# Performance work log

Measured on AMD Instinct MI355X. Metric: run time of the kernel, lower is better.

## Reference

```python
import jax, jax.numpy as jnp
import numpy as np

B, T, E, H = 2, 2048, 1024, 16
D = E // H            # head dim = 64
ROT = D // 2          # rotary_dim = 32 (only first half of head dim is rotated)
THETA = 10000.0


def _rope(x):
    # x: (B, H, T, D). Faithful to rotary_embedding_torch.rotate_queries_or_keys
    # with dim=ROT: rotate first ROT features, interleaved-pair style, pass rest.
    t = x.shape[-2]
    inv = 1.0 / (THETA ** (jnp.arange(0, ROT, 2, dtype=jnp.float32) / ROT))   # (ROT//2,)
    freqs = jnp.arange(t, dtype=jnp.float32)[:, None] * inv[None, :]          # (T, ROT//2)
    freqs = jnp.repeat(freqs, 2, axis=-1)                                      # (T, ROT)
    cos, sin = jnp.cos(freqs), jnp.sin(freqs)
    xr, xp = x[..., :ROT], x[..., ROT:]
    p = xr.reshape(*xr.shape[:-1], ROT // 2, 2)
    rot = jnp.stack((-p[..., 1], p[..., 0]), axis=-1).reshape(xr.shape)
    return jnp.concatenate([xr * cos + rot * sin, xp], axis=-1)


def setup_inputs() -> dict:
    key = jax.random.key(0)
    k1, k2, k3 = jax.random.split(key, 3)
    query = jax.random.normal(k1, (B, T, E), dtype=jnp.float32)
    inputs = {
        "query": query,
        "key": query,            # ignored (cross_attention=False)
        "value": query,          # ignored
        "padding_mask": jnp.ones((B, T), dtype=bool),
        "in_proj_weight": jax.random.uniform(k2, (3 * E, E), dtype=jnp.float32),
        "out_proj_weight": jax.random.normal(k3, (E, E), dtype=jnp.float32) * (E ** -0.5),
    }
    return inputs


def reference(query, key, value, padding_mask, in_proj_weight, out_proj_weight):
    # cross_attention=False: key/value are overwritten by query
    key = query
    value = query
    q = query @ in_proj_weight[:E].T
    k = key @ in_proj_weight[E:2 * E].T
    v = value @ in_proj_weight[2 * E:].T
    # NOTE: raw reshape (B,T,E)->(B,H,T,D), exactly as in the torch module
    q = q.reshape(B, H, T, D)
    k = k.reshape(B, H, T, D)
    v = v.reshape(B, H, T, D)
    q = _rope(q)
    k = _rope(k)   # causal self-attention path: rotate keys too
    causal = jnp.tril(jnp.ones((T, T), dtype=bool))                 # (T, T)
    mask = causal[None, None] & padding_mask[:, None, None, :]      # (B,1,T,T) -> broadcast over H
    scores = jnp.einsum("bhqd,bhkd->bhqk", q, k) / jnp.sqrt(jnp.float32(D))
    scores = jnp.where(mask, scores, -jnp.inf)
    attn = jax.nn.softmax(scores, axis=-1)
    x = jnp.einsum("bhqk,bhkd->bhqd", attn, v)
    x = x.reshape(B, T, E)      # raw reshape back, as in torch
    return x @ out_proj_weight.T
```

## Files before the change

kernel.cpp:

```cpp
#include <hip/hip_runtime.h>
#include <stdint.h>

#define T_ 2048
#define E_ 1024

typedef __attribute__((ext_vector_type(8))) __bf16 bf16x8;
typedef __attribute__((ext_vector_type(4))) float f32x4;

__device__ __forceinline__ void gload_lds16(const void* g, void* l) {
  __builtin_amdgcn_global_load_lds(
      (const __attribute__((address_space(1))) unsigned int*)g,
      (__attribute__((address_space(3))) unsigned int*)l, 16, 0, 0);
}

__global__ __launch_bounds__(256) void k_prep(const float4* __restrict__ q,
                                              ushort4* __restrict__ xh,
                                              ushort4* __restrict__ xl,
                                              const float4* __restrict__ win,
                                              ushort4* __restrict__ whh,
                                              ushort4* __restrict__ whl,
                                              const float4* __restrict__ wout,
                                              ushort4* __restrict__ wob,
                                              float2* __restrict__ cs) {
  const int b = blockIdx.x, tid = threadIdx.x;
  if (b < 7168) {
    const float4* src;
    ushort4 *hi, *lo;
    int i;
    if (b < 4096) { src = q; hi = xh; lo = xl; i = b * 256 + tid; }
    else          { src = win; hi = whh; lo = whl; i = (b - 4096) * 256 + tid; }
    float4 x = src[i];
    float xs[4] = {x.x, x.y, x.z, x.w};
    union { __bf16 bb[4]; ushort4 u; } H, L;
#pragma unroll
    for (int jj = 0; jj < 4; ++jj) {
      __bf16 h = (__bf16)xs[jj];
      H.bb[jj] = h;
      L.bb[jj] = (__bf16)(xs[jj] - (float)h);
    }
    hi[i] = H.u;
    lo[i] = L.u;
  } else if (b < 8192) {
    int i = (b - 7168) * 256 + tid;
    float4 x = wout[i];
    float xs[4] = {x.x, x.y, x.z, x.w};
    union { __bf16 bb[4]; ushort4 u; } H;
#pragma unroll
    for (int jj = 0; jj < 4; ++jj) H.bb[jj] = (__bf16)xs[jj];
    wob[i] = H.u;
  } else {
    int i = (b - 8192) * 256 + tid;
    int t = i >> 4, f = i & 15;
    double inv = pow(10000.0, -(double)f / 16.0);
    double ang = (double)t * inv;
    cs[i] = make_float2((float)cos(ang), (float)sin(ang));
  }
}

template <int EPI, bool HILO>
__global__ __launch_bounds__(256) void k_gemm(const __bf16* __restrict__ Ah,
                                              const __bf16* __restrict__ Al,
                                              const __bf16* __restrict__ Bh,
                                              const __bf16* __restrict__ Bl,
                                              int M, int N, int K,
                                              const float2* __restrict__ cs,
                                              __bf16* __restrict__ qhi,
                                              __bf16* __restrict__ qlo,
                                              __bf16* __restrict__ khi,
                                              __bf16* __restrict__ klo,
                                              __bf16* __restrict__ v16,
                                              float* __restrict__ C32) {
  __shared__ __align__(16) __bf16 AsH[128 * 32];
  __shared__ __align__(16) __bf16 BsH[128 * 32];
  __shared__ __align__(16) __bf16 AsL[HILO ? 128 * 32 : 4];
  __shared__ __align__(16) __bf16 BsL[HILO ? 128 * 32 : 4];
  const int tid = threadIdx.x, lane = tid & 63, w = tid >> 6;
  const int wm = w >> 1, wn = w & 1;
  const int g = lane >> 4, d = lane & 15;
  const int m0 = blockIdx.y * 128, n0 = blockIdx.x * 128;

  f32x4 acc[4][4];
#pragma unroll
  for (int i = 0; i < 4; ++i)
#pragma unroll
    for (int j = 0; j < 4; ++j) acc[i][j] = (f32x4)(0.0f);

  const int row0 = tid >> 2, kc = tid & 3;
  const int row1 = 64 + row0;

  for (int k0 = 0; k0 < K; k0 += 32) {
    __syncthreads();
    gload_lds16(Ah + (size_t)(m0 + row0) * K + k0 + kc * 8, &AsH[w * 512]);
    gload_lds16(Ah + (size_t)(m0 + row1) * K + k0 + kc * 8, &AsH[2048 + w * 512]);
    gload_lds16(Bh + (size_t)(n0 + row0) * K + k0 + kc * 8, &BsH[w * 512]);
    gload_lds16(Bh + (size_t)(n0 + row1) * K + k0 + kc * 8, &BsH[2048 + w * 512]);
    if constexpr (HILO) {
      gload_lds16(Al + (size_t)(m0 + row0) * K + k0 + kc * 8, &AsL[w * 512]);
      gload_lds16(Al + (size_t)(m0 + row1) * K + k0 + kc * 8, &AsL[2048 + w * 512]);
      gload_lds16(Bl + (size_t)(n0 + row0) * K + k0 + kc * 8, &BsL[w * 512]);
      gload_lds16(Bl + (size_t)(n0 + row1) * K + k0 + kc * 8, &BsL[2048 + w * 512]);
    }
    __syncthreads();
    bf16x8 ah[4], bh[4], al[4], bl[4];
#pragma unroll
    for (int i = 0; i < 4; ++i) {
      ah[i] = *(const bf16x8*)&AsH[(wm * 64 + i * 16 + d) * 32 + g * 8];
      bh[i] = *(const bf16x8*)&BsH[(wn * 64 + i * 16 + d) * 32 + g * 8];
      if constexpr (HILO) {
        al[i] = *(const bf16x8*)&AsL[(wm * 64 + i * 16 + d) * 32 + g * 8];
        bl[i] = *(const bf16x8*)&BsL[(wn * 64 + i * 16 + d) * 32 + g * 8];
      }
    }
#pragma unroll
    for (int i = 0; i < 4; ++i)
#pragma unroll
      for (int j = 0; j < 4; ++j) {
        acc[i][j] = __builtin_amdgcn_mfma_f32_16x16x32_bf16(ah[i], bh[j], acc[i][j], 0, 0, 0);
        if constexpr (HILO) {
          acc[i][j] = __builtin_amdgcn_mfma_f32_16x16x32_bf16(al[i], bh[j], acc[i][j], 0, 0, 0);
          acc[i][j] = __builtin_amdgcn_mfma_f32_16x16x32_bf16(ah[i], bl[j], acc[i][j], 0, 0, 0);
        }
      }
  }

#pragma unroll
  for (int i = 0; i < 4; ++i) {
    const int rbase = m0 + wm * 64 + i * 16 + g * 4;
#pragma unroll
    for (int j = 0; j < 4; ++j) {
      const int col = n0 + wn * 64 + j * 16 + d;
#pragma unroll
      for (int r = 0; r < 4; ++r) {
        const float vv = acc[i][j][r];
        const int row = rbase + r;
        if constexpr (EPI == 0) {
          const float xp = __shfl_xor(vv, 1);
          const int which = col >> 10;
          const int cl = col & 1023;
          const int d2 = cl & 63;
          const int t2 = (row & 127) * 16 + (cl >> 6);
          float y;
          if (d2 < 32) {
            const float2 cse = cs[t2 * 16 + (d2 >> 1)];
            y = (d2 & 1) ? (vv * cse.x + xp * cse.y) : (vv * cse.x - xp * cse.y);
          } else {
            y = vv;
          }
          if (which == 0) y *= 0.18033688011112042f;
          const __bf16 hi = (__bf16)y;
          const __bf16 lo = (__bf16)(y - (float)hi);
          const size_t off = (size_t)row * 1024 + cl;
          (which ? khi : qhi)[off] = hi;
          (which ? klo : qlo)[off] = lo;
        } else if constexpr (EPI == 1) {
          C32[(size_t)row * N + col] = vv;
        } else {
          v16[(size_t)row * N + col] = (__bf16)vv;
        }
      }
    }
  }
}

template <int EPI>
__global__ __launch_bounds__(256) void k_gemm64(const __bf16* __restrict__ Ah,
                                                const __bf16* __restrict__ Bh,
                                                int M, int N, int K,
                                                __bf16* __restrict__ v16,
                                                float* __restrict__ C32) {
  __shared__ __align__(16) __bf16 As[64 * 32];
  __shared__ __align__(16) __bf16 Bs[128 * 32];
  const int tid = threadIdx.x, lane = tid & 63, w = tid >> 6;
  const int g = lane >> 4, d = lane & 15;
  const int m0 = blockIdx.y * 64, n0 = blockIdx.x * 128;

  f32x4 acc[4][2];
#pragma unroll
  for (int i = 0; i < 4; ++i)
#pragma unroll
    for (int j = 0; j < 2; ++j) acc[i][j] = (f32x4)(0.0f);

  const int row0 = tid >> 2, kc = tid & 3;
  const int row1 = 64 + row0;

  for (int k0 = 0; k0 < K; k0 += 32) {
    __syncthreads();
    gload_lds16(Ah + (size_t)(m0 + row0) * K + k0 + kc * 8, &As[w * 512]);
    gload_lds16(Bh + (size_t)(n0 + row0) * K + k0 + kc * 8, &Bs[w * 512]);
    gload_lds16(Bh + (size_t)(n0 + row1) * K + k0 + kc * 8, &Bs[2048 + w * 512]);
    __syncthreads();
    bf16x8 ah[4], bh[2];
#pragma unroll
    for (int i = 0; i < 4; ++i) ah[i] = *(const bf16x8*)&As[(i * 16 + d) * 32 + g * 8];
#pragma unroll
    for (int j = 0; j < 2; ++j)
      bh[j] = *(const bf16x8*)&Bs[(w * 32 + j * 16 + d) * 32 + g * 8];
#pragma unroll
    for (int i = 0; i < 4; ++i)
#pragma unroll
      for (int j = 0; j < 2; ++j)
        acc[i][j] = __builtin_amdgcn_mfma_f32_16x16x32_bf16(ah[i], bh[j], acc[i][j], 0, 0, 0);
  }

#pragma unroll
  for (int i = 0; i < 4; ++i) {
    const int rbase = m0 + i * 16 + g * 4;
#pragma unroll
    for (int j = 0; j < 2; ++j) {
      const int col = n0 + w * 32 + j * 16 + d;
#pragma unroll
      for (int r = 0; r < 4; ++r) {
        const int row = rbase + r;
        if constexpr (EPI == 1) C32[(size_t)row * N + col] = acc[i][j][r];
        else v16[(size_t)row * N + col] = (__bf16)acc[i][j][r];
      }
    }
  }
}

__global__ __launch_bounds__(256) void k_vtrans(const __bf16* __restrict__ v16,
                                                __bf16* __restrict__ v16t) {
  __shared__ __bf16 TB[64][72];
  const int p = blockIdx.y, t0 = blockIdx.x * 64;
  const int tid = threadIdx.x;
  const int r = tid >> 2, c4 = (tid & 3) * 16;
  const __bf16* src = v16 + ((size_t)p * 2048 + t0 + r) * 64 + c4;
  bf16x8 A = *(const bf16x8*)src;
  bf16x8 B2 = *(const bf16x8*)(src + 8);
#pragma unroll
  for (int e = 0; e < 8; ++e) {
    TB[c4 + e][r] = A[e];
    TB[c4 + 8 + e][r] = B2[e];
  }
  __syncthreads();
  const int dd = tid >> 2, cc = (tid & 3) * 16;
  __bf16* dst = v16t + ((size_t)p * 64 + dd) * 2048 + t0 + cc;
  *(bf16x8*)dst = *(const bf16x8*)&TB[dd][cc];
  *(bf16x8*)(dst + 8) = *(const bf16x8*)&TB[dd][cc + 8];
}

__global__ __launch_bounds__(512, 4) void k_attn(const __bf16* __restrict__ qhi,
                                                 const __bf16* __restrict__ qlo,
                                                 const __bf16* __restrict__ khi,
                                                 const __bf16* __restrict__ klo,
                                                 const __bf16* __restrict__ v16t,
                                                 __bf16* __restrict__ x16,
                                                 float* __restrict__ po,
                                                 float* __restrict__ pm,
                                                 float* __restrict__ pl_) {
  __shared__ __align__(16) __bf16 KH[2][64 * 64];
  __shared__ __align__(16) __bf16 KL[2][64 * 64];
  __shared__ __align__(16) __bf16 VT[2][64 * 64];
  __shared__ __align__(16) __bf16 PL[8][16 * 72];

  const int b = blockIdx.x, panel = blockIdx.y;
  const int u0 = 9 * b;
  int qtA = 0;
  while (2 * (qtA + 1) * (qtA + 2) <= u0) ++qtA;
  const int cumA = 2 * qtA * (qtA + 1);
  const int cumB = 2 * (qtA + 1) * (qtA + 2);
  const int jloA = u0 - cumA;
  const bool two = (u0 + 9 > cumB);
  const int jhiA = two ? (cumB - 1 - cumA) : (u0 + 8 - cumA);
  const int jhiB = u0 + 8 - cumB;

  const int tid = threadIdx.x, lane = tid & 63, w = tid >> 6;
  const int g = lane >> 4, d = lane & 15;
  const size_t hb = (size_t)panel * T_ * 64;

  const int kr = tid >> 3, kc = tid & 7;
  const int swz = (kc ^ (kr & 7)) * 8;
  const __bf16* kB = khi + hb;
  const __bf16* lB = klo + hb;
  const __bf16* vB = v16t + (size_t)panel * (64 * T_);

#define STAGE(j, bb)                                                        \
  {                                                                         \
    gload_lds16(kB + (size_t)((j) * 64 + kr) * 64 + swz, &KH[bb][w * 512]); \
    gload_lds16(lB + (size_t)((j) * 64 + kr) * 64 + swz, &KL[bb][w * 512]); \
    gload_lds16(vB + (size_t)kr * T_ + (j) * 64 + swz, &VT[bb][w * 512]);   \
  }

  int cur = 0;
  STAGE(jloA, 0);

  for (int seg = 0; seg < 2; ++seg) {
    if (seg && !two) break;
    const int qt = qtA + seg;
    const int jlo = seg ? 0 : jloA;
    const int jhi = seg ? jhiB : jhiA;
    const int q0 = qt << 8;

    bf16x8 qh[2][2], ql[2][2];
#pragma unroll
    for (int rb = 0; rb < 2; ++rb) {
      const int rbi = w * 2 + rb;
      const size_t qrow = hb + (size_t)(q0 + rbi * 16 + d) * 64;
      qh[rb][0] = *(const bf16x8*)&qhi[qrow + g * 8];
      qh[rb][1] = *(const bf16x8*)&qhi[qrow + 32 + g * 8];
      ql[rb][0] = *(const bf16x8*)&qlo[qrow + g * 8];
      ql[rb][1] = *(const bf16x8*)&qlo[qrow + 32 + g * 8];
    }

    f32x4 o[2][4];
#pragma unroll
    for (int rb = 0; rb < 2; ++rb)
#pragma unroll
      for (int i = 0; i < 4; ++i) o[rb][i] = (f32x4)(0.0f);
    float m_[2] = {-__builtin_inff(), -__builtin_inff()};
    float l_[2] = {0.0f, 0.0f};

    for (int j = jlo; j <= jhi; ++j) {
      __syncthreads();
      if (j < jhi) {
        STAGE(j + 1, cur ^ 1);
      } else if (!seg && two) {
        STAGE(0, cur ^ 1);
      }

#pragma unroll
      for (int rb = 0; rb < 2; ++rb) {
        const int rbi = w * 2 + rb;
        const int qrow0 = q0 + rbi * 16;
        if (j * 64 > qrow0 + 15) continue;

        f32x4 s[4];
        __builtin_amdgcn_s_setprio(1);
#pragma unroll
        for (int f = 0; f < 4; ++f) {
          f32x4 accs = (f32x4)(0.0f);
          const int colr = f * 16 + d;
#pragma unroll
          for (int ds = 0; ds < 2; ++ds) {
            const int slot = ((ds * 4 + g) ^ (colr & 7)) * 8;
            const bf16x8 kf = *(const bf16x8*)&KH[cur][colr * 64 + slot];
            const bf16x8 lf = *(const bf16x8*)&KL[cur][colr * 64 + slot];
            accs = __builtin_amdgcn_mfma_f32_16x16x32_bf16(kf, qh[rb][ds], accs, 0, 0, 0);
            accs = __builtin_amdgcn_mfma_f32_16x16x32_bf16(kf, ql[rb][ds], accs, 0, 0, 0);
            accs = __builtin_amdgcn_mfma_f32_16x16x32_bf16(lf, qh[rb][ds], accs, 0, 0, 0);
          }
          s[f] = accs;
        }
        __builtin_amdgcn_s_setprio(0);

        if (j * 64 + 63 > qrow0) {
          const int qq = qrow0 + d;
#pragma unroll
          for (int f = 0; f < 4; ++f)
#pragma unroll
            for (int r = 0; r < 4; ++r) {
              const int kv = j * 64 + f * 16 + g * 4 + r;
              if (kv > qq) s[f][r] = -30000.0f;
            }
        }

        float pmax = fmaxf(fmaxf(s[0][0], s[0][1]), fmaxf(s[0][2], s[0][3]));
#pragma unroll
        for (int f = 1; f < 4; ++f)
          pmax = fmaxf(pmax, fmaxf(fmaxf(s[f][0], s[f][1]), fmaxf(s[f][2], s[f][3])));
        pmax = fmaxf(pmax, __shfl_xor(pmax, 16));
        pmax = fmaxf(pmax, __shfl_xor(pmax, 32));

        if (!__all(pmax - m_[rb] <= 11.5f)) {
          const float mnew = fmaxf(m_[rb], pmax);
          const float fac = exp2f(m_[rb] - mnew);
          m_[rb] = mnew;
          float facr[4];
#pragma unroll
          for (int r = 0; r < 4; ++r)
            facr[r] = __shfl(fac, (lane & 48) | (g * 4 + r));
#pragma unroll
          for (int ni = 0; ni < 4; ++ni)
#pragma unroll
            for (int r = 0; r < 4; ++r) o[rb][ni][r] *= facr[r];
          l_[rb] *= fac;
        }

        float sum = 0.0f;
#pragma unroll
        for (int f = 0; f < 4; ++f) {
          union { __bf16 bb[4]; ushort4 u4; } pk;
#pragma unroll
          for (int r = 0; r < 4; ++r) {
            const float pv = exp2f(s[f][r] - m_[rb]);
            sum += pv;
            pk.bb[r] = (__bf16)pv;
          }
          *(ushort4*)&PL[w][d * 72 + f * 16 + g * 4] = pk.u4;
        }
        sum += __shfl_xor(sum, 16);
        sum += __shfl_xor(sum, 32);
        l_[rb] += sum;

        __builtin_amdgcn_s_setprio(1);
#pragma unroll
        for (int ks = 0; ks < 2; ++ks) {
          const bf16x8 pa = *(const bf16x8*)&PL[w][d * 72 + ks * 32 + g * 8];
#pragma unroll
          for (int ni = 0; ni < 4; ++ni) {
            const bf16x8 vf =
                *(const bf16x8*)&VT[cur][(ni * 16 + d) * 64 + (((ks * 4 + g) ^ (d & 7)) * 8)];
            o[rb][ni] = __builtin_amdgcn_mfma_f32_16x16x32_bf16(pa, vf, o[rb][ni], 0, 0, 0);
          }
        }
        __builtin_amdgcn_s_setprio(0);
      }
      cur ^= 1;
    }

    if (jlo == 0 && jhi == 4 * qt + 3) {
#pragma unroll
      for (int rb = 0; rb < 2; ++rb) {
        const int rbi = w * 2 + rb;
        float lr[4];
#pragma unroll
        for (int r = 0; r < 4; ++r)
          lr[r] = __shfl(l_[rb], (lane & 48) | (g * 4 + r));
#pragma unroll
        for (int ni = 0; ni < 4; ++ni)
#pragma unroll
          for (int r = 0; r < 4; ++r) {
            const size_t row = hb + (size_t)(q0 + rbi * 16 + g * 4 + r) * 64;
            x16[row + ni * 16 + d] = (__bf16)(o[rb][ni][r] / lr[r]);
          }
      }
    } else {
      const int slot = panel * 23 + b + qt;
#pragma unroll
      for (int rb = 0; rb < 2; ++rb) {
        const int rbi = w * 2 + rb;
#pragma unroll
        for (int ni = 0; ni < 4; ++ni)
#pragma unroll
          for (int r = 0; r < 4; ++r) {
            const int rowin = rbi * 16 + g * 4 + r;
            po[(size_t)slot * 16384 + rowin * 64 + ni * 16 + d] = o[rb][ni][r];
          }
        if (g == 0) {
          pm[slot * 256 + rbi * 16 + d] = m_[rb];
          pl_[slot * 256 + rbi * 16 + d] = l_[rb];
        }
      }
    }
  }
#undef STAGE
}

__global__ __launch_bounds__(256) void k_combine(const float* __restrict__ po,
                                                 const float* __restrict__ pm,
                                                 const float* __restrict__ pl_,
                                                 __bf16* __restrict__ x16) {
  const int p = blockIdx.y;
  const int li = blockIdx.x * 256 + threadIdx.x;
  const int d = li & 63;
  const int t2 = 256 + (li >> 6);
  const int qt = t2 >> 8;
  const int rowin = t2 & 255;
  const int cq = 2 * qt * (qt + 1);
  const int nc = (cq + 4 * qt + 3) / 9 - cq / 9 + 1;
  const int s0 = p * 23 + cq / 9 + qt;
  float M = -__builtin_inff();
  for (int s = 0; s < nc; ++s) M = fmaxf(M, pm[(s0 + s) * 256 + rowin]);
  float L = 0.0f, O = 0.0f;
  for (int s = 0; s < nc; ++s) {
    const float ww = exp2f(pm[(s0 + s) * 256 + rowin] - M);
    L += pl_[(s0 + s) * 256 + rowin] * ww;
    O += po[(size_t)(s0 + s) * 16384 + rowin * 64 + d] * ww;
  }
  x16[((size_t)p * T_ + t2) * 64 + d] = (__bf16)(O / L);
}

extern "C" void kernel_launch(void* const* d_in, const int* in_sizes, int n_in,
                              void* d_out, int out_size, void* d_ws, size_t ws_size,
                              hipStream_t stream) {
  const float* query = (const float*)d_in[0];
  const float* win = (const float*)d_in[4];
  const float* wout = (const float*)d_in[5];
  float* out = (float*)d_out;

  const size_t MB = 1024 * 1024;
  const size_t KB = 1024;
  char* ws = (char*)d_ws;
  __bf16* xh = (__bf16*)(ws);
  __bf16* xl = (__bf16*)(ws + 8 * MB);
  __bf16* whh = (__bf16*)(ws + 16 * MB);
  __bf16* whl = (__bf16*)(ws + 22 * MB);
  __bf16* wob = (__bf16*)(ws + 28 * MB);
  float* pm = (float*)(ws + 30 * MB);
  float* pl_ = (float*)(ws + 30 * MB + 768 * KB);
  float2* cs = (float2*)(ws + 31 * MB + 512 * KB);
  float* po = (float*)(ws + 32 * MB);
  __bf16* qhi = (__bf16*)(ws + 78 * MB);
  __bf16* qlo = (__bf16*)(ws + 86 * MB);
  __bf16* khi = (__bf16*)(ws + 94 * MB);
  __bf16* klo = (__bf16*)(ws + 102 * MB);
  __bf16* x16 = (__bf16*)(ws + 78 * MB);
  __bf16* v16 = (__bf16*)(ws + 64 * MB);
  __bf16* v16t = (__bf16*)(ws);

  k_prep<<<8320, 256, 0, stream>>>((const float4*)query, (ushort4*)xh, (ushort4*)xl,
                                   (const float4*)win, (ushort4*)whh, (ushort4*)whl,
                                   (const float4*)wout, (ushort4*)wob, cs);

  dim3 gqk(16, 32);
  k_gemm<0, true><<<gqk, 256, 0, stream>>>(xh, xl, whh, whl, 4096, 2048, 1024, cs,
                                           qhi, qlo, khi, klo, nullptr, nullptr);
  dim3 gv(8, 64);
  k_gemm64<2><<<gv, 256, 0, stream>>>(xh, whh + (size_t)2048 * 1024, 4096, 1024, 1024,
                                      v16, nullptr);

  dim3 gt(32, 32);
  k_vtrans<<<gt, 256, 0, stream>>>(v16, v16t);

  dim3 ga(16, 32);
  k_attn<<<ga, 512, 0, stream>>>(qhi, qlo, khi, klo, v16t, x16, po, pm, pl_);

  dim3 gc(448, 32);
  k_combine<<<gc, 256, 0, stream>>>(po, pm, pl_, x16);

  dim3 go(8, 64);
  k_gemm64<1><<<go, 256, 0, stream>>>(x16, wob, 4096, 1024, 1024, nullptr, out);
}
```

Measured before the change: 204.7 us.

## Widen GEMM K-tile to 64 with XOR-swizzled LDS and fuse V transpose

```diff
diff --git a/kernel.cpp b/kernel.cpp
--- a/kernel.cpp
+++ b/kernel.cpp
@@ -57,23 +57,20 @@
   }
 }
 
-template <int EPI, bool HILO>
-__global__ __launch_bounds__(256) void k_gemm(const __bf16* __restrict__ Ah,
-                                              const __bf16* __restrict__ Al,
-                                              const __bf16* __restrict__ Bh,
-                                              const __bf16* __restrict__ Bl,
-                                              int M, int N, int K,
-                                              const float2* __restrict__ cs,
-                                              __bf16* __restrict__ qhi,
-                                              __bf16* __restrict__ qlo,
-                                              __bf16* __restrict__ khi,
-                                              __bf16* __restrict__ klo,
-                                              __bf16* __restrict__ v16,
-                                              float* __restrict__ C32) {
-  __shared__ __align__(16) __bf16 AsH[128 * 32];
-  __shared__ __align__(16) __bf16 BsH[128 * 32];
-  __shared__ __align__(16) __bf16 AsL[HILO ? 128 * 32 : 4];
-  __shared__ __align__(16) __bf16 BsL[HILO ? 128 * 32 : 4];
+__global__ __launch_bounds__(256) void k_gemmqk(const __bf16* __restrict__ Ah,
+                                                const __bf16* __restrict__ Al,
+                                                const __bf16* __restrict__ Bh,
+                                                const __bf16* __restrict__ Bl,
+                                                int K,
+                                                const float2* __restrict__ cs,
+                                                __bf16* __restrict__ qhi,
+                                                __bf16* __restrict__ qlo,
+                                                __bf16* __restrict__ khi,
+                                                __bf16* __restrict__ klo) {
+  __shared__ __align__(16) __bf16 AsH[128 * 64];
+  __shared__ __align__(16) __bf16 BsH[128 * 64];
+  __shared__ __align__(16) __bf16 AsL[128 * 64];
+  __shared__ __align__(16) __bf16 BsL[128 * 64];
   const int tid = threadIdx.x, lane = tid & 63, w = tid >> 6;
   const int wm = w >> 1, wn = w & 1;
   const int g = lane >> 4, d = lane & 15;
@@ -85,42 +82,45 @@
 #pragma unroll
     for (int j = 0; j < 4; ++j) acc[i][j] = (f32x4)(0.0f);
 
-  const int row0 = tid >> 2, kc = tid & 3;
-  const int row1 = 64 + row0;
-
-  for (int k0 = 0; k0 < K; k0 += 32) {
+  const int lr8 = lane >> 3;
+  const int swz8 = ((lane & 7) ^ lr8) * 8;
+  const int rsl = (d & 7);
+
+  for (int k0 = 0; k0 < K; k0 += 64) {
     __syncthreads();
-    gload_lds16(Ah + (size_t)(m0 + row0) * K + k0 + kc * 8, &AsH[w * 512]);
-    gload_lds16(Ah + (size_t)(m0 + row1) * K + k0 + kc * 8, &AsH[2048 + w * 512]);
-    gload_lds16(Bh + (size_t)(n0 + row0) * K + k0 + kc * 8, &BsH[w * 512]);
-    gload_lds16(Bh + (size_t)(n0 + row1) * K + k0 + kc * 8, &BsH[2048 + w * 512]);
-    if constexpr (HILO) {
-      gload_lds16(Al + (size_t)(m0 + row0) * K + k0 + kc * 8, &AsL[w * 512]);
-      gload_lds16(Al + (size_t)(m0 + row1) * K + k0 + kc * 8, &AsL[2048 + w * 512]);
-      gload_lds16(Bl + (size_t)(n0 + row0) * K + k0 + kc * 8, &BsL[w * 512]);
-      gload_lds16(Bl + (size_t)(n0 + row1) * K + k0 + kc * 8, &BsL[2048 + w * 512]);
+#pragma unroll
+    for (int c = 0; c < 4; ++c) {
+      const int rr = c * 32 + w * 8 + lr8;
+      const int ldo = (c * 32 + w * 8) * 64;
+      gload_lds16(Ah + (size_t)(m0 + rr) * K + k0 + swz8, &AsH[ldo]);
+      gload_lds16(Al + (size_t)(m0 + rr) * K + k0 + swz8, &AsL[ldo]);
+      gload_lds16(Bh + (size_t)(n0 + rr) * K + k0 + swz8, &BsH[ldo]);
+      gload_lds16(Bl + (size_t)(n0 + rr) * K + k0 + swz8, &BsL[ldo]);
     }
     __syncthreads();
-    bf16x8 ah[4], bh[4], al[4], bl[4];
-#pragma unroll
-    for (int i = 0; i < 4; ++i) {
-      ah[i] = *(const bf16x8*)&AsH[(wm * 64 + i * 16 + d) * 32 + g * 8];
-      bh[i] = *(const bf16x8*)&BsH[(wn * 64 + i * 16 + d) * 32 + g * 8];
-      if constexpr (HILO) {
-        al[i] = *(const bf16x8*)&AsL[(wm * 64 + i * 16 + d) * 32 + g * 8];
-        bl[i] = *(const bf16x8*)&BsL[(wn * 64 + i * 16 + d) * 32 + g * 8];
-      }
-    }
-#pragma unroll
-    for (int i = 0; i < 4; ++i)
+#pragma unroll
+    for (int k2 = 0; k2 < 2; ++k2) {
+      const int sl = ((k2 * 4 + g) ^ rsl) * 8;
+      bf16x8 bh[4], bl[4];
 #pragma unroll
       for (int j = 0; j < 4; ++j) {
-        acc[i][j] = __builtin_amdgcn_mfma_f32_16x16x32_bf16(ah[i], bh[j], acc[i][j], 0, 0, 0);
-        if constexpr (HILO) {
-          acc[i][j] = __builtin_amdgcn_mfma_f32_16x16x32_bf16(al[i], bh[j], acc[i][j], 0, 0, 0);
-          acc[i][j] = __builtin_amdgcn_mfma_f32_16x16x32_bf16(ah[i], bl[j], acc[i][j], 0, 0, 0);
-        }
-      }
+        const int r = wn * 64 + j * 16 + d;
+        bh[j] = *(const bf16x8*)&BsH[r * 64 + sl];
+        bl[j] = *(const bf16x8*)&BsL[r * 64 + sl];
+      }
+#pragma unroll
+      for (int i = 0; i < 4; ++i) {
+        const int r = wm * 64 + i * 16 + d;
+        const bf16x8 ahf = *(const bf16x8*)&AsH[r * 64 + sl];
+        const bf16x8 alf = *(const bf16x8*)&AsL[r * 64 + sl];
+#pragma unroll
+        for (int j = 0; j < 4; ++j) {
+          acc[i][j] = __builtin_amdgcn_mfma_f32_16x16x32_bf16(ahf, bh[j], acc[i][j], 0, 0, 0);
+          acc[i][j] = __builtin_amdgcn_mfma_f32_16x16x32_bf16(alf, bh[j], acc[i][j], 0, 0, 0);
+          acc[i][j] = __builtin_amdgcn_mfma_f32_16x16x32_bf16(ahf, bl[j], acc[i][j], 0, 0, 0);
+        }
+      }
+    }
   }
 
 #pragma unroll
@@ -133,30 +133,24 @@
       for (int r = 0; r < 4; ++r) {
         const float vv = acc[i][j][r];
         const int row = rbase + r;
-        if constexpr (EPI == 0) {
-          const float xp = __shfl_xor(vv, 1);
-          const int which = col >> 10;
-          const int cl = col & 1023;
-          const int d2 = cl & 63;
-          const int t2 = (row & 127) * 16 + (cl >> 6);
-          float y;
-          if (d2 < 32) {
-            const float2 cse = cs[t2 * 16 + (d2 >> 1)];
-            y = (d2 & 1) ? (vv * cse.x + xp * cse.y) : (vv * cse.x - xp * cse.y);
-          } else {
-            y = vv;
-          }
-          if (which == 0) y *= 0.18033688011112042f;
-          const __bf16 hi = (__bf16)y;
-          const __bf16 lo = (__bf16)(y - (float)hi);
-          const size_t off = (size_t)row * 1024 + cl;
-          (which ? khi : qhi)[off] = hi;
-          (which ? klo : qlo)[off] = lo;
-        } else if constexpr (EPI == 1) {
-          C32[(size_t)row * N + col] = vv;
+        const float xp = __shfl_xor(vv, 1);
+        const int which = col >> 10;
+        const int cl = col & 1023;
+        const int d2 = cl & 63;
+        const int t2 = (row & 127) * 16 + (cl >> 6);
+        float y;
+        if (d2 < 32) {
+          const float2 cse = cs[t2 * 16 + (d2 >> 1)];
+          y = (d2 & 1) ? (vv * cse.x + xp * cse.y) : (vv * cse.x - xp * cse.y);
         } else {
-          v16[(size_t)row * N + col] = (__bf16)vv;
-        }
+          y = vv;
+        }
+        if (which == 0) y *= 0.18033688011112042f;
+        const __bf16 hi = (__bf16)y;
+        const __bf16 lo = (__bf16)(y - (float)hi);
+        const size_t off = (size_t)row * 1024 + cl;
+        (which ? khi : qhi)[off] = hi;
+        (which ? klo : qlo)[off] = lo;
       }
     }
   }
@@ -165,11 +159,11 @@
 template <int EPI>
 __global__ __launch_bounds__(256) void k_gemm64(const __bf16* __restrict__ Ah,
                                                 const __bf16* __restrict__ Bh,
-                                                int M, int N, int K,
-                                                __bf16* __restrict__ v16,
+                                                int N, int K,
+                                                __bf16* __restrict__ vt,
                                                 float* __restrict__ C32) {
-  __shared__ __align__(16) __bf16 As[64 * 32];
-  __shared__ __align__(16) __bf16 Bs[128 * 32];
+  __shared__ __align__(16) __bf16 As[64 * 64];
+  __shared__ __align__(16) __bf16 Bs[128 * 64];
   const int tid = threadIdx.x, lane = tid & 63, w = tid >> 6;
   const int g = lane >> 4, d = lane & 15;
   const int m0 = blockIdx.y * 64, n0 = blockIdx.x * 128;
@@ -180,26 +174,39 @@
 #pragma unroll
     for (int j = 0; j < 2; ++j) acc[i][j] = (f32x4)(0.0f);
 
-  const int row0 = tid >> 2, kc = tid & 3;
-  const int row1 = 64 + row0;
-
-  for (int k0 = 0; k0 < K; k0 += 32) {
+  const int lr8 = lane >> 3;
+  const int swz8 = ((lane & 7) ^ lr8) * 8;
+  const int rsl = (d & 7);
+
+  for (int k0 = 0; k0 < K; k0 += 64) {
     __syncthreads();
-    gload_lds16(Ah + (size_t)(m0 + row0) * K + k0 + kc * 8, &As[w * 512]);
-    gload_lds16(Bh + (size_t)(n0 + row0) * K + k0 + kc * 8, &Bs[w * 512]);
-    gload_lds16(Bh + (size_t)(n0 + row1) * K + k0 + kc * 8, &Bs[2048 + w * 512]);
+#pragma unroll
+    for (int c = 0; c < 2; ++c) {
+      const int rr = c * 32 + w * 8 + lr8;
+      gload_lds16(Ah + (size_t)(m0 + rr) * K + k0 + swz8, &As[(c * 32 + w * 8) * 64]);
+    }
+#pragma unroll
+    for (int c = 0; c < 4; ++c) {
+      const int rr = c * 32 + w * 8 + lr8;
+      gload_lds16(Bh + (size_t)(n0 + rr) * K + k0 + swz8, &Bs[(c * 32 + w * 8) * 64]);
+    }
     __syncthreads();
-    bf16x8 ah[4], bh[2];
-#pragma unroll
-    for (int i = 0; i < 4; ++i) ah[i] = *(const bf16x8*)&As[(i * 16 + d) * 32 + g * 8];
-#pragma unroll
-    for (int j = 0; j < 2; ++j)
-      bh[j] = *(const bf16x8*)&Bs[(w * 32 + j * 16 + d) * 32 + g * 8];
-#pragma unroll
-    for (int i = 0; i < 4; ++i)
+#pragma unroll
+    for (int k2 = 0; k2 < 2; ++k2) {
+      const int sl = ((k2 * 4 + g) ^ rsl) * 8;
+      bf16x8 bh[2], ah[4];
 #pragma unroll
       for (int j = 0; j < 2; ++j)
-        acc[i][j] = __builtin_amdgcn_mfma_f32_16x16x32_bf16(ah[i], bh[j], acc[i][j], 0, 0, 0);
+        bh[j] = *(const bf16x8*)&Bs[(w * 32 + j * 16 + d) * 64 + sl];
+#pragma unroll
+      for (int i = 0; i < 4; ++i)
+        ah[i] = *(const bf16x8*)&As[(i * 16 + d) * 64 + sl];
+#pragma unroll
+      for (int i = 0; i < 4; ++i)
+#pragma unroll
+        for (int j = 0; j < 2; ++j)
+          acc[i][j] = __builtin_amdgcn_mfma_f32_16x16x32_bf16(ah[i], bh[j], acc[i][j], 0, 0, 0);
+    }
   }
 
 #pragma unroll
@@ -211,32 +218,17 @@
 #pragma unroll
       for (int r = 0; r < 4; ++r) {
         const int row = rbase + r;
-        if constexpr (EPI == 1) C32[(size_t)row * N + col] = acc[i][j][r];
-        else v16[(size_t)row * N + col] = (__bf16)acc[i][j][r];
-      }
-    }
-  }
-}
-
-__global__ __launch_bounds__(256) void k_vtrans(const __bf16* __restrict__ v16,
-                                                __bf16* __restrict__ v16t) {
-  __shared__ __bf16 TB[64][72];
-  const int p = blockIdx.y, t0 = blockIdx.x * 64;
-  const int tid = threadIdx.x;
-  const int r = tid >> 2, c4 = (tid & 3) * 16;
-  const __bf16* src = v16 + ((size_t)p * 2048 + t0 + r) * 64 + c4;
-  bf16x8 A = *(const bf16x8*)src;
-  bf16x8 B2 = *(const bf16x8*)(src + 8);
-#pragma unroll
-  for (int e = 0; e < 8; ++e) {
-    TB[c4 + e][r] = A[e];
-    TB[c4 + 8 + e][r] = B2[e];
-  }
-  __syncthreads();
-  const int dd = tid >> 2, cc = (tid & 3) * 16;
-  __bf16* dst = v16t + ((size_t)p * 64 + dd) * 2048 + t0 + cc;
-  *(bf16x8*)dst = *(const bf16x8*)&TB[dd][cc];
-  *(bf16x8*)(dst + 8) = *(const bf16x8*)&TB[dd][cc + 8];
+        if constexpr (EPI == 1) {
+          C32[(size_t)row * N + col] = acc[i][j][r];
+        } else {
+          const int p = row >> 7;
+          const int tp = ((row & 127) << 4) | (col >> 6);
+          const int dp = col & 63;
+          vt[((size_t)p * 64 + dp) * 2048 + tp] = (__bf16)acc[i][j][r];
+        }
+      }
+    }
+  }
 }
 
 __global__ __launch_bounds__(512, 4) void k_attn(const __bf16* __restrict__ qhi,
@@ -483,6 +475,7 @@
   char* ws = (char*)d_ws;
   __bf16* xh = (__bf16*)(ws);
   __bf16* xl = (__bf16*)(ws + 8 * MB);
+  __bf16* v16t = (__bf16*)(ws + 8 * MB);
   __bf16* whh = (__bf16*)(ws + 16 * MB);
   __bf16* whl = (__bf16*)(ws + 22 * MB);
   __bf16* wob = (__bf16*)(ws + 28 * MB);
@@ -495,22 +488,17 @@
   __bf16* khi = (__bf16*)(ws + 94 * MB);
   __bf16* klo = (__bf16*)(ws + 102 * MB);
   __bf16* x16 = (__bf16*)(ws + 78 * MB);
-  __bf16* v16 = (__bf16*)(ws + 64 * MB);
-  __bf16* v16t = (__bf16*)(ws);
 
   k_prep<<<8320, 256, 0, stream>>>((const float4*)query, (ushort4*)xh, (ushort4*)xl,
                                    (const float4*)win, (ushort4*)whh, (ushort4*)whl,
                                    (const float4*)wout, (ushort4*)wob, cs);
 
   dim3 gqk(16, 32);
-  k_gemm<0, true><<<gqk, 256, 0, stream>>>(xh, xl, whh, whl, 4096, 2048, 1024, cs,
-                                           qhi, qlo, khi, klo, nullptr, nullptr);
+  k_gemmqk<<<gqk, 256, 0, stream>>>(xh, xl, whh, whl, 1024, cs, qhi, qlo, khi, klo);
+
   dim3 gv(8, 64);
-  k_gemm64<2><<<gv, 256, 0, stream>>>(xh, whh + (size_t)2048 * 1024, 4096, 1024, 1024,
-                                      v16, nullptr);
-
-  dim3 gt(32, 32);
-  k_vtrans<<<gt, 256, 0, stream>>>(v16, v16t);
+  k_gemm64<2><<<gv, 256, 0, stream>>>(xh, whh + (size_t)2048 * 1024, 1024, 1024,
+                                      v16t, nullptr);
 
   dim3 ga(16, 32);
   k_attn<<<ga, 512, 0, stream>>>(qhi, qlo, khi, klo, v16t, x16, po, pm, pl_);
@@ -519,5 +507,5 @@
   k_combine<<<gc, 256, 0, stream>>>(po, pm, pl_, x16);
 
   dim3 go(8, 64);
-  k_gemm64<1><<<go, 256, 0, stream>>>(x16, wob, 4096, 1024, 1024, nullptr, out);
-}
+  k_gemm64<1><<<go, 256, 0, stream>>>(x16, wob, 1024, 1024, nullptr, out);
+}
```

New measurement: 204.8 us. About the same (+0.0%).
